# Optimization experiments

Hardware: AMD Instinct MI355X
Metric: run time of the kernel (lower is better)

Reference implementation:

```python
import jax, jax.numpy as jnp
import numpy as np

# Config (from Mamba3Config defaults)
D_MODEL = 768
EXPAND = 4
D_INNER = EXPAND * D_MODEL          # 3072
D_HEAD = 64
N_HEADS = D_INNER // D_HEAD         # 48
N_EXPERTS = 8
TOP_K = 2
R3 = 256                            # latent MoE input dim
R2 = 1024                           # latent MoE output dim
EPS = 1e-5
TANH_SCALE = 10.0                   # fast_scaled_tanh default
ROUTER_TEMP = 0.5                   # get_router_temperature(step=None) -> t_end


def _rms_norm(x, w):
    return x * jax.lax.rsqrt(jnp.mean(x * x, axis=-1, keepdims=True) + EPS) * w


def _scaled_tanh(x):
    return TANH_SCALE * jnp.tanh(x * (1.0 / TANH_SCALE))


def setup_inputs() -> dict:
    key = jax.random.key(0)
    ks = jax.random.split(key, 13)
    s = 0.02
    B, L = 2, 4096
    return {
        "x": jax.random.normal(ks[0], (B, L, D_MODEL), dtype=jnp.float32),
        "rms1_w": jnp.ones((D_MODEL,), jnp.float32),
        "W_in": s * jax.random.normal(ks[1], (D_MODEL, 2 * D_INNER + N_HEADS), jnp.float32),
        "dt_bias": jax.random.uniform(ks[2], (N_HEADS,), jnp.float32, -4.0, -1.0),  # dt in [dt_min, dt_max]-ish
        "W_out": s * jax.random.normal(ks[3], (D_INNER, D_MODEL), jnp.float32),
        "ls1": 0.01 * jnp.ones((D_MODEL,), jnp.float32),
        "rms2_w": jnp.ones((D_MODEL,), jnp.float32),
        "W_down": s * jax.random.normal(ks[4], (D_MODEL, R3), jnp.float32),
        "W_router": s * jax.random.normal(ks[5], (D_MODEL, N_EXPERTS), jnp.float32),
        "G": s * jax.random.normal(ks[6], (N_EXPERTS, R3, R2), jnp.float32),
        "W_up": s * jax.random.normal(ks[7], (R2, D_MODEL), jnp.float32),
        "ls2": 0.01 * jnp.ones((D_MODEL,), jnp.float32),
    }


def reference(x, rms1_w, W_in, dt_bias, W_out, ls1, rms2_w, W_down, W_router, G, W_up, ls2):
    B, L, _ = x.shape
    # ---- Mamba selective-scan branch ----
    xn = _rms_norm(x, rms1_w)
    proj = xn @ W_in                                   # [B,L,2*Di+H]
    u, z, dt = jnp.split(proj, [D_INNER, 2 * D_INNER], axis=-1)
    log_alpha = -jax.nn.softplus(dt + dt_bias)         # [B,L,H], per-head scalar decay
    alpha = jnp.exp(log_alpha)[..., None]              # [B,L,H,1]
    u4 = u.reshape(B, L, N_HEADS, D_HEAD)

    def combine(left, right):                          # first_order_combine_op
        a_l, b_l = left
        a_r, b_r = right
        return (a_r * a_l, a_r * b_l + b_r)

    _, h = jax.lax.associative_scan(
        combine, (jnp.broadcast_to(alpha, u4.shape), u4), axis=1)
    y = h.reshape(B, L, D_INNER) * jax.nn.silu(z)
    y = _scaled_tanh(y)
    x1 = x + ls1 * (y @ W_out)

    # ---- Fused latent MoE (Tucker) branch ----
    x2n = _rms_norm(x1, rms2_w)
    lat = _scaled_tanh(x2n @ W_down)                   # [B,L,r3]
    logits = (x2n @ W_router) * (1.0 / ROUTER_TEMP)    # [B,L,E]
    vals, idx = jax.lax.top_k(logits, TOP_K)
    probs = jax.nn.softmax(vals, axis=-1)              # [B,L,K]
    # dense combine weights: w[b,l,e] = sum_k probs_k * [idx_k == e]
    w = jnp.sum(jax.nn.one_hot(idx, N_EXPERTS, dtype=lat.dtype) * probs[..., None], axis=-2)
    # out[b,l,c] = sum_e w[b,l,e] * (lat[b,l,:] @ G[e])  (== fused gather grouped-GEMM)
    moe = jnp.einsum('blr,erc,ble->blc', lat, G, w)    # [B,L,r2]
    out = x1 + ls2 * (moe @ W_up)
    return out
```

## Files before the change

### kernel.cpp

```cpp
#include <hip/hip_runtime.h>
#include <stdint.h>

typedef unsigned short ushort_t;
typedef __attribute__((ext_vector_type(8))) __bf16 bf16x8;
typedef __attribute__((ext_vector_type(4))) float floatx4;
typedef __attribute__((ext_vector_type(8))) unsigned short ushort8v;

#define TT 8192L
#define LB 4096L
#define DD 768L
#define DI 3072L
#define NH 48L
#define R3C 256L
#define R2C 1024L
#define NP 6272L
#define CHS 64L

__device__ __forceinline__ float b2f(ushort_t u) {
  union { unsigned u32; float f; } v; v.u32 = ((unsigned)u) << 16; return v.f;
}
__device__ __forceinline__ ushort_t f2b(float f) {
  union { float f; unsigned u32; } v; v.f = f;
  unsigned r = v.u32 + 0x7FFFu + ((v.u32 >> 16) & 1u);
  return (ushort_t)(r >> 16);
}
__device__ __forceinline__ float fast_tanh(float x) {
  float e = __expf(2.0f * x);
  return 1.0f - 2.0f / (e + 1.0f);
}
__device__ __forceinline__ void g2l16(const void* g, void* l) {
  __builtin_amdgcn_global_load_lds(
      (const __attribute__((address_space(1))) unsigned int*)g,
      (__attribute__((address_space(3))) unsigned int*)l, 16, 0, 0);
}

__global__ __launch_bounds__(256) void k_prep(const float* __restrict__ s0, ushort_t* __restrict__ d0,
                                              const float* __restrict__ s1, ushort_t* __restrict__ d1,
                                              const float* __restrict__ s2, ushort_t* __restrict__ d2,
                                              const float* __restrict__ s3, ushort_t* __restrict__ d3,
                                              const float* __restrict__ s4, ushort_t* __restrict__ d4,
                                              const float* __restrict__ x,
                                              const float* __restrict__ w1,
                                              ushort_t* __restrict__ xn) {
  __shared__ float tile[64][65];
  int id = blockIdx.x;
  if (id < 2504) {
    const float* src; ushort_t* dst; int K, N, gx;
    if (id < 1176)      {            src = s0; dst = d0; K = 768;  N = 6192; gx = 12; }
    else if (id < 1752) { id -= 1176; src = s1; dst = d1; K = 3072; N = 768;  gx = 48; }
    else if (id < 1800) { id -= 1752; src = s2; dst = d2; K = 768;  N = 256;  gx = 12; }
    else if (id < 1992) { id -= 1800; src = s3; dst = d3; K = 1024; N = 768;  gx = 16; }
    else                { id -= 1992; src = s4; dst = d4; K = 2048; N = 1024; gx = 32; }
    int k0 = (id % gx) * 64, n0 = (id / gx) * 64;
    int c = threadIdx.x & 63, r4 = threadIdx.x >> 6;
#pragma unroll
    for (int s = 0; s < 16; s++) {
      int r = s * 4 + r4;
      int n = n0 + c;
      tile[c][r] = (n < N) ? src[(long)(k0 + r) * N + n] : 0.0f;
    }
    __syncthreads();
#pragma unroll
    for (int s = 0; s < 16; s++) {
      int r = s * 4 + r4;
      dst[(long)(n0 + r) * K + k0 + c] = f2b(tile[r][c]);
    }
  } else {
    int t = id - 2504, tid = threadIdx.x;
    int lane = tid & 63, wid = tid >> 6;
    const float* xr = x + (long)t * DD;
    float v0 = xr[tid], v1 = xr[tid + 256], v2 = xr[tid + 512];
    float ss = v0 * v0 + v1 * v1 + v2 * v2;
    for (int o = 32; o; o >>= 1) ss += __shfl_down(ss, o);
    __shared__ float red[4];
    if (lane == 0) red[wid] = ss;
    __syncthreads();
    float tot = red[0] + red[1] + red[2] + red[3];
    float rr = rsqrtf(tot / 768.0f + 1e-5f);
    ushort_t* orow = xn + (long)t * DD;
    orow[tid]       = f2b(v0 * rr * w1[tid]);
    orow[tid + 256] = f2b(v1 * rr * w1[tid + 256]);
    orow[tid + 512] = f2b(v2 * rr * w1[tid + 512]);
  }
}

__global__ __launch_bounds__(256) void k_fuse2(const float* __restrict__ P,
                                               const float* __restrict__ x,
                                               const float* __restrict__ ls1,
                                               const float* __restrict__ w2,
                                               const float* __restrict__ wr,
                                               ushort_t* __restrict__ x1,
                                               ushort_t* __restrict__ x2n,
                                               float* __restrict__ wrt) {
  int t = blockIdx.x, tid = threadIdx.x;
  int lane = tid & 63, wid = tid >> 6;
  int dd[3] = {tid, tid + 256, tid + 512};
  float v[3];
#pragma unroll
  for (int i = 0; i < 3; i++) {
    long ix = (long)t * DD + dd[i];
    float s = P[ix] + P[LB * DD + ix] + P[2 * LB * DD + ix] + P[3 * LB * DD + ix];
    float xv = x[ix] + ls1[dd[i]] * s;
    x1[ix] = f2b(xv);
    v[i] = xv;
  }
  float ss = v[0] * v[0] + v[1] * v[1] + v[2] * v[2];
  for (int o = 32; o; o >>= 1) ss += __shfl_down(ss, o);
  __shared__ float red[4];
  __shared__ float wred[4][8];
  __shared__ float slog[8];
  if (lane == 0) red[wid] = ss;
  __syncthreads();
  float tot = red[0] + red[1] + red[2] + red[3];
  float rr = rsqrtf(tot / 768.0f + 1e-5f);
  float p[8] = {0, 0, 0, 0, 0, 0, 0, 0};
  ushort_t* orow = x2n + (long)t * DD;
#pragma unroll
  for (int i = 0; i < 3; i++) {
    float xnv = v[i] * rr * w2[dd[i]];
    orow[dd[i]] = f2b(xnv);
    const float* wrow = wr + (long)dd[i] * 8;
#pragma unroll
    for (int e = 0; e < 8; e++) p[e] += xnv * wrow[e];
  }
#pragma unroll
  for (int e = 0; e < 8; e++) {
    float s = p[e];
    for (int o = 32; o; o >>= 1) s += __shfl_down(s, o);
    if (lane == 0) wred[wid][e] = s;
  }
  __syncthreads();
  if (tid < 8)
    slog[tid] = (wred[0][tid] + wred[1][tid] + wred[2][tid] + wred[3][tid]) * 2.0f;
  __syncthreads();
  if (tid == 0) {
    float l[8];
#pragma unroll
    for (int e = 0; e < 8; e++) l[e] = slog[e];
    int e0 = 0; float b0 = l[0];
#pragma unroll
    for (int e = 1; e < 8; e++) if (l[e] > b0) { b0 = l[e]; e0 = e; }
    int e1 = -1; float b1 = -1e30f;
#pragma unroll
    for (int e = 0; e < 8; e++) if (e != e0 && l[e] > b1) { b1 = l[e]; e1 = e; }
    float ex = __expf(b1 - b0);
    float pd = 1.0f / (1.0f + ex);
    float* wo = wrt + (long)t * 8;
#pragma unroll
    for (int e = 0; e < 8; e++) wo[e] = 0.0f;
    wo[e0] = pd;
    wo[e1] = ex * pd;
  }
}

__device__ __forceinline__ void stage_tile(const ushort_t* __restrict__ g, long rowstride,
                                           ushort_t* __restrict__ lds, int lane) {
  const int lrow = lane >> 3;
  const int dcol = (lane & 7) * 8;
#pragma unroll
  for (int c8 = 0; c8 < 8; c8++) {
    ushort8v v = *(const ushort8v*)(g + (long)(c8 * 8 + lrow) * rowstride + dcol);
    *(ushort8v*)&lds[(c8 * 64 + lane) * 8] = v;
  }
}

__device__ __forceinline__ float alpha_of(const ushort_t* __restrict__ proj, int tok, int h,
                                          const float* __restrict__ dtb) {
  float dt = b2f(proj[(long)tok * NP + 2 * DI + h]) + dtb[h];
  float sp = (dt > 20.0f) ? dt : log1pf(__expf(dt));
  return __expf(-sp);
}

__global__ __launch_bounds__(64) void k_scan1(const ushort_t* __restrict__ proj,
                                              const float* __restrict__ dtb,
                                              float* __restrict__ ssum,
                                              float* __restrict__ asum) {
  __shared__ __align__(16) ushort_t u_lds[64 * 64];
  __shared__ float s_alpha[64];
  const int lane = threadIdx.x;
  const int idx = blockIdx.x;
  const int c = idx & 63;
  const int h = idx >> 6;
  s_alpha[lane] = alpha_of(proj, (int)(c * CHS) + lane, h, dtb);
  const ushort_t* ug = proj + (long)c * CHS * NP + (long)h * 64;
  stage_tile(ug, NP, u_lds, lane);
  __syncthreads();
  float s = 0.0f, A = 1.0f;
#pragma unroll
  for (int tt = 0; tt < 64; tt++) {
    float a = s_alpha[tt];
    float u = b2f(u_lds[tt * 64 + lane]);
    s = fmaf(a, s, u);
    A *= a;
  }
  ssum[(long)idx * 64 + lane] = s;
  if (lane == 0) asum[idx] = A;
}

__global__ __launch_bounds__(64) void k_scan3(const ushort_t* __restrict__ proj,
                                              const float* __restrict__ dtb,
                                              const float* __restrict__ ssum,
                                              const float* __restrict__ asum,
                                              ushort_t* __restrict__ y) {
  __shared__ __align__(16) ushort_t u_lds[64 * 64];
  __shared__ __align__(16) ushort_t z_lds[64 * 64];
  __shared__ float s_alpha[64];
  const int lane = threadIdx.x;
  const int idx = blockIdx.x;
  const int c = idx & 63;
  const int h = idx >> 6;
  s_alpha[lane] = alpha_of(proj, (int)(c * CHS) + lane, h, dtb);
  const ushort_t* ug = proj + (long)c * CHS * NP + (long)h * 64;
  const ushort_t* zg = ug + DI;
  ushort_t* yg = y + (long)c * CHS * DI + (long)h * 64;
  stage_tile(ug, NP, u_lds, lane);
  stage_tile(zg, NP, z_lds, lane);
  float hs = 0.0f;
  for (int cc = 0; cc < c; cc++) {
    float A = asum[h * 64 + cc];
    float s = ssum[((long)(h * 64 + cc)) * 64 + lane];
    hs = fmaf(A, hs, s);
  }
  __syncthreads();
#pragma unroll
  for (int tt = 0; tt < 64; tt++) {
    float a = s_alpha[tt];
    float u = b2f(u_lds[tt * 64 + lane]);
    hs = fmaf(a, hs, u);
    float zv = b2f(z_lds[tt * 64 + lane]);
    float sig = 1.0f / (1.0f + __expf(-zv));
    float yv = hs * zv * sig;
    yv = 10.0f * fast_tanh(yv * 0.1f);
    yg[(long)tt * DI + lane] = f2b(yv);
  }
}

__global__ __launch_bounds__(256) void k_moe_in(const float* __restrict__ P,
                                                const float* __restrict__ wrt,
                                                ushort_t* __restrict__ abig) {
  int t = blockIdx.x, d = threadIdx.x;
  __shared__ float sw[8];
  if (d < 8) sw[d] = wrt[(long)t * 8 + d];
  long ix = (long)t * R3C + d;
  float s = P[ix] + P[TT * R3C + ix] + P[2 * TT * R3C + ix];
  __syncthreads();
  float lv = 10.0f * fast_tanh(0.1f * s);
  ushort_t* ab = abig + (long)t * 2048;
#pragma unroll
  for (int e = 0; e < 8; e++) ab[e * 256 + d] = f2b(sw[e] * lv);
}

template <int MODE>
__global__ __launch_bounds__(256, 4) void k_gemm(const ushort_t* __restrict__ A,
                                                 const ushort_t* __restrict__ Bt,
                                                 void* __restrict__ Cout, int K, int kstride,
                                                 int ldc, long zoff) {
  __shared__ __align__(16) ushort_t sA[2 * 128 * 32];
  __shared__ __align__(16) ushort_t sB[2 * 128 * 32];
  const int tid = threadIdx.x;
  const int lane = tid & 63, wid = tid >> 6;
  const int lm = lane & 15, q = lane >> 4;
  const int wm = wid >> 1, wn = wid & 1;
  const long row0 = (long)blockIdx.x * 128;
  const long col0 = (long)blockIdx.y * 128;
  const int z = blockIdx.z;
  A += (long)z * K;
  Bt += (long)z * K;

  floatx4 acc[4][4] = {};

  const int trow = tid >> 2;
  const int tcol = (tid & 3) * 8;
  const ushort_t* Ag = A + (row0 + trow) * (long)kstride + tcol;
  const ushort_t* Bg = Bt + (col0 + trow) * (long)kstride + tcol;
  const long rstep = 64L * kstride;

  for (int k0 = 0; k0 < K; k0 += 64) {
#pragma unroll
    for (int kk = 0; kk < 2; kk++)
#pragma unroll
      for (int rh = 0; rh < 2; rh++) {
        g2l16(Ag + rh * rstep + k0 + kk * 32, sA + kk * 4096 + rh * 2048 + wid * 512);
        g2l16(Bg + rh * rstep + k0 + kk * 32, sB + kk * 4096 + rh * 2048 + wid * 512);
      }
    __syncthreads();
#pragma unroll
    for (int kk = 0; kk < 2; kk++) {
      bf16x8 af[4], bfr[4];
#pragma unroll
      for (int i = 0; i < 4; i++)
        af[i] = *(const bf16x8*)(const void*)&sA[kk * 4096 + (wm * 64 + i * 16 + lm) * 32 + q * 8];
#pragma unroll
      for (int j = 0; j < 4; j++)
        bfr[j] = *(const bf16x8*)(const void*)&sB[kk * 4096 + (wn * 64 + j * 16 + lm) * 32 + q * 8];
#pragma unroll
      for (int i = 0; i < 4; i++)
#pragma unroll
        for (int j = 0; j < 4; j++)
          acc[i][j] = __builtin_amdgcn_mfma_f32_16x16x32_bf16(af[i], bfr[j], acc[i][j], 0, 0, 0);
    }
    __syncthreads();
  }

  if (MODE == 0) {
    ushort_t* ep = ((wid & 2) ? sB : sA) + (wid & 1) * 2304;
    ushort_t* Cb = (ushort_t*)Cout;
    const int rr = lane >> 3, cc = (lane & 7) * 8;
    __syncthreads();
#pragma unroll
    for (int p = 0; p < 2; p++) {
#pragma unroll
      for (int i2 = 0; i2 < 2; i2++)
#pragma unroll
        for (int j = 0; j < 4; j++)
#pragma unroll
          for (int r = 0; r < 4; r++)
            ep[(i2 * 16 + q * 4 + r) * 72 + j * 16 + lm] = f2b(acc[p * 2 + i2][j][r]);
#pragma unroll
      for (int s = 0; s < 4; s++) {
        ushort8v vv = *(const ushort8v*)&ep[(s * 8 + rr) * 72 + cc];
        long grow = row0 + wm * 64 + p * 32 + s * 8 + rr;
        *(ushort8v*)&Cb[grow * (long)ldc + col0 + wn * 64 + cc] = vv;
      }
    }
  } else {
#pragma unroll
    for (int i = 0; i < 4; i++) {
#pragma unroll
      for (int r = 0; r < 4; r++) {
        long row = row0 + wm * 64 + i * 16 + q * 4 + r;
#pragma unroll
        for (int j = 0; j < 4; j++) {
          long col = col0 + wn * 64 + j * 16 + lm;
          ((float*)Cout)[(long)z * zoff + row * (long)ldc + col] = acc[i][j][r];
        }
      }
    }
  }
}

__global__ __launch_bounds__(256) void k_comb_out(const float* __restrict__ P, long zoff, int nz,
                                                  const ushort_t* __restrict__ x1,
                                                  const float* __restrict__ ls,
                                                  float* __restrict__ outp) {
  long i = ((long)blockIdx.x * 256 + threadIdx.x) * 4;
  float s[4] = {0, 0, 0, 0};
  for (int zz = 0; zz < nz; zz++) {
    const float* p = P + (long)zz * zoff + i;
#pragma unroll
    for (int j = 0; j < 4; j++) s[j] += p[j];
  }
  int c = (int)(i % DD);
#pragma unroll
  for (int j = 0; j < 4; j++) outp[i + j] = b2f(x1[i + j]) + ls[c + j] * s[j];
}

#define OFF_WINT   0L
#define OFF_WOUTT  9633792L
#define OFF_WDNT   14352384L
#define OFF_WUPT   14745600L
#define OFF_GT     16318464L
#define OFF_X1     20512768L
#define OFF_WRT    33095680L
#define OFF_SSUM   34144256L
#define OFF_ASUM   34930688L
#define OFF_XN     35729408L
#define OFF_Y      48312320L
#define OFF_PROJ   73478144L
#define OFF_X2N    OFF_XN
#define OFF_PART   OFF_PROJ
#define OFF_DPART  OFF_Y
#define OFF_ABIG   OFF_PROJ
#define OFF_MOE    OFF_Y
#define OFF_UPART  OFF_PROJ
#define WS_NEEDED  124858368L

extern "C" void kernel_launch(void* const* d_in, const int* in_sizes, int n_in,
                              void* d_out, int out_size, void* d_ws, size_t ws_size,
                              hipStream_t stream) {
  const float* x     = (const float*)d_in[0];
  const float* rms1w = (const float*)d_in[1];
  const float* W_in  = (const float*)d_in[2];
  const float* dtb   = (const float*)d_in[3];
  const float* W_out = (const float*)d_in[4];
  const float* ls1   = (const float*)d_in[5];
  const float* rms2w = (const float*)d_in[6];
  const float* W_dn  = (const float*)d_in[7];
  const float* W_rtr = (const float*)d_in[8];
  const float* G     = (const float*)d_in[9];
  const float* W_up  = (const float*)d_in[10];
  const float* ls2   = (const float*)d_in[11];
  if (ws_size < (size_t)WS_NEEDED) return;

  char* ws = (char*)d_ws;
  ushort_t* W_inT  = (ushort_t*)(ws + OFF_WINT);
  ushort_t* W_outT = (ushort_t*)(ws + OFF_WOUTT);
  ushort_t* W_dnT  = (ushort_t*)(ws + OFF_WDNT);
  ushort_t* W_upT  = (ushort_t*)(ws + OFF_WUPT);
  ushort_t* GT     = (ushort_t*)(ws + OFF_GT);
  ushort_t* x1     = (ushort_t*)(ws + OFF_X1);
  float*    wrt    = (float*)(ws + OFF_WRT);
  float*    ssum   = (float*)(ws + OFF_SSUM);
  float*    asum   = (float*)(ws + OFF_ASUM);
  ushort_t* xn     = (ushort_t*)(ws + OFF_XN);
  ushort_t* y      = (ushort_t*)(ws + OFF_Y);
  ushort_t* proj   = (ushort_t*)(ws + OFF_PROJ);
  float*    part   = (float*)(ws + OFF_PART);
  float*    dpart  = (float*)(ws + OFF_DPART);
  ushort_t* abig   = (ushort_t*)(ws + OFF_ABIG);
  ushort_t* moe    = (ushort_t*)(ws + OFF_MOE);
  float*    upart  = (float*)(ws + OFF_UPART);
  ushort_t* x2n    = (ushort_t*)(ws + OFF_X2N);
  float*    outp   = (float*)d_out;

  k_prep<<<10696, 256, 0, stream>>>(W_in, W_inT, W_out, W_outT, W_dn, W_dnT,
                                    W_up, W_upT, G, GT, x, rms1w, xn);

  for (int b = 0; b < 2; b++) {
    const ushort_t* xnb = xn + (long)b * LB * DD;
    k_gemm<0><<<dim3(32, 49, 1), 256, 0, stream>>>(xnb, W_inT, proj, 768, 768, (int)NP, 0);
    k_scan1<<<3072, 64, 0, stream>>>(proj, dtb, ssum, asum);
    k_scan3<<<3072, 64, 0, stream>>>(proj, dtb, ssum, asum, y);
    k_gemm<4><<<dim3(32, 6, 4), 256, 0, stream>>>(y, W_outT, part, 768, 3072, 768, LB * DD);
    k_fuse2<<<4096, 256, 0, stream>>>(part, x + (long)b * LB * DD, ls1, rms2w, W_rtr,
                                      x1 + (long)b * LB * DD, x2n + (long)b * LB * DD,
                                      wrt + (long)b * LB * 8);
  }

  k_gemm<4><<<dim3(64, 2, 3), 256, 0, stream>>>(x2n, W_dnT, dpart, 256, 768, 256, TT * R3C);
  k_moe_in<<<8192, 256, 0, stream>>>(dpart, wrt, abig);
  k_gemm<0><<<dim3(64, 8, 1), 256, 0, stream>>>(abig, GT, moe, 2048, 2048, 1024, 0);
  k_gemm<4><<<dim3(64, 6, 2), 256, 0, stream>>>(moe, W_upT, upart, 512, 1024, 768, TT * DD);
  k_comb_out<<<6144, 256, 0, stream>>>(upart, TT * DD, 2, x1, ls2, outp);
}
```

Baseline: 534.0 us.

## Store split-K partials as bf16 and add a separate chunk-carry scan kernel

Split-K GEMM partial outputs are now written as bf16 through the LDS-staged vectorized epilogue instead of scattered fp32 stores, and the consumers (fuse2, moe_in, comb_out) read bf16. This halves partial-buffer traffic and gives coalesced stores. Separately, the per-block serial loop over earlier chunks in scan3, which costs O(c) work per block, is replaced by a small k_scan2 kernel that precomputes carries per head. Summing bf16-rounded partials loses some precision, and the change adds one extra launch per batch.

```diff
diff --git a/kernel.cpp b/kernel.cpp
--- a/kernel.cpp
+++ b/kernel.cpp
@@ -4,6 +4,7 @@
 typedef unsigned short ushort_t;
 typedef __attribute__((ext_vector_type(8))) __bf16 bf16x8;
 typedef __attribute__((ext_vector_type(4))) float floatx4;
+typedef __attribute__((ext_vector_type(4))) unsigned short ushort4v;
 typedef __attribute__((ext_vector_type(8))) unsigned short ushort8v;
 
 #define TT 8192L
@@ -84,7 +85,7 @@
   }
 }
 
-__global__ __launch_bounds__(256) void k_fuse2(const float* __restrict__ P,
+__global__ __launch_bounds__(256) void k_fuse2(const ushort_t* __restrict__ P,
                                                const float* __restrict__ x,
                                                const float* __restrict__ ls1,
                                                const float* __restrict__ w2,
@@ -99,7 +100,7 @@
 #pragma unroll
   for (int i = 0; i < 3; i++) {
     long ix = (long)t * DD + dd[i];
-    float s = P[ix] + P[LB * DD + ix] + P[2 * LB * DD + ix] + P[3 * LB * DD + ix];
+    float s = b2f(P[ix]) + b2f(P[LB * DD + ix]) + b2f(P[2 * LB * DD + ix]) + b2f(P[3 * LB * DD + ix]);
     float xv = x[ix] + ls1[dd[i]] * s;
     x1[ix] = f2b(xv);
     v[i] = xv;
@@ -197,10 +198,22 @@
   if (lane == 0) asum[idx] = A;
 }
 
+__global__ __launch_bounds__(64) void k_scan2(const float* __restrict__ ssum,
+                                              const float* __restrict__ asum,
+                                              float* __restrict__ carry) {
+  int h = blockIdx.x, lane = threadIdx.x;
+  float cv = 0.0f;
+  for (int c = 0; c < 64; c++) {
+    carry[((long)h * 64 + c) * 64 + lane] = cv;
+    float A = asum[h * 64 + c];
+    float s = ssum[((long)h * 64 + c) * 64 + lane];
+    cv = A * cv + s;
+  }
+}
+
 __global__ __launch_bounds__(64) void k_scan3(const ushort_t* __restrict__ proj,
                                               const float* __restrict__ dtb,
-                                              const float* __restrict__ ssum,
-                                              const float* __restrict__ asum,
+                                              const float* __restrict__ carry,
                                               ushort_t* __restrict__ y) {
   __shared__ __align__(16) ushort_t u_lds[64 * 64];
   __shared__ __align__(16) ushort_t z_lds[64 * 64];
@@ -215,13 +228,8 @@
   ushort_t* yg = y + (long)c * CHS * DI + (long)h * 64;
   stage_tile(ug, NP, u_lds, lane);
   stage_tile(zg, NP, z_lds, lane);
-  float hs = 0.0f;
-  for (int cc = 0; cc < c; cc++) {
-    float A = asum[h * 64 + cc];
-    float s = ssum[((long)(h * 64 + cc)) * 64 + lane];
-    hs = fmaf(A, hs, s);
-  }
-  __syncthreads();
+  __syncthreads();
+  float hs = carry[(long)idx * 64 + lane];
 #pragma unroll
   for (int tt = 0; tt < 64; tt++) {
     float a = s_alpha[tt];
@@ -235,14 +243,14 @@
   }
 }
 
-__global__ __launch_bounds__(256) void k_moe_in(const float* __restrict__ P,
+__global__ __launch_bounds__(256) void k_moe_in(const ushort_t* __restrict__ P,
                                                 const float* __restrict__ wrt,
                                                 ushort_t* __restrict__ abig) {
   int t = blockIdx.x, d = threadIdx.x;
   __shared__ float sw[8];
   if (d < 8) sw[d] = wrt[(long)t * 8 + d];
   long ix = (long)t * R3C + d;
-  float s = P[ix] + P[TT * R3C + ix] + P[2 * TT * R3C + ix];
+  float s = b2f(P[ix]) + b2f(P[TT * R3C + ix]) + b2f(P[2 * TT * R3C + ix]);
   __syncthreads();
   float lv = 10.0f * fast_tanh(0.1f * s);
   ushort_t* ab = abig + (long)t * 2048;
@@ -250,10 +258,9 @@
   for (int e = 0; e < 8; e++) ab[e * 256 + d] = f2b(sw[e] * lv);
 }
 
-template <int MODE>
 __global__ __launch_bounds__(256, 4) void k_gemm(const ushort_t* __restrict__ A,
                                                  const ushort_t* __restrict__ Bt,
-                                                 void* __restrict__ Cout, int K, int kstride,
+                                                 ushort_t* __restrict__ C, int K, int kstride,
                                                  int ldc, long zoff) {
   __shared__ __align__(16) ushort_t sA[2 * 128 * 32];
   __shared__ __align__(16) ushort_t sB[2 * 128 * 32];
@@ -302,53 +309,37 @@
     __syncthreads();
   }
 
-  if (MODE == 0) {
-    ushort_t* ep = ((wid & 2) ? sB : sA) + (wid & 1) * 2304;
-    ushort_t* Cb = (ushort_t*)Cout;
-    const int rr = lane >> 3, cc = (lane & 7) * 8;
-    __syncthreads();
-#pragma unroll
-    for (int p = 0; p < 2; p++) {
-#pragma unroll
-      for (int i2 = 0; i2 < 2; i2++)
-#pragma unroll
-        for (int j = 0; j < 4; j++)
-#pragma unroll
-          for (int r = 0; r < 4; r++)
-            ep[(i2 * 16 + q * 4 + r) * 72 + j * 16 + lm] = f2b(acc[p * 2 + i2][j][r]);
-#pragma unroll
-      for (int s = 0; s < 4; s++) {
-        ushort8v vv = *(const ushort8v*)&ep[(s * 8 + rr) * 72 + cc];
-        long grow = row0 + wm * 64 + p * 32 + s * 8 + rr;
-        *(ushort8v*)&Cb[grow * (long)ldc + col0 + wn * 64 + cc] = vv;
-      }
+  ushort_t* ep = ((wid & 2) ? sB : sA) + (wid & 1) * 2304;
+  ushort_t* Cb = C + (long)z * zoff;
+  const int rr = lane >> 3, cc = (lane & 7) * 8;
+  __syncthreads();
+#pragma unroll
+  for (int p = 0; p < 2; p++) {
+#pragma unroll
+    for (int i2 = 0; i2 < 2; i2++)
+#pragma unroll
+      for (int j = 0; j < 4; j++)
+#pragma unroll
+        for (int r = 0; r < 4; r++)
+          ep[(i2 * 16 + q * 4 + r) * 72 + j * 16 + lm] = f2b(acc[p * 2 + i2][j][r]);
+#pragma unroll
+    for (int s = 0; s < 4; s++) {
+      ushort8v vv = *(const ushort8v*)&ep[(s * 8 + rr) * 72 + cc];
+      long grow = row0 + wm * 64 + p * 32 + s * 8 + rr;
+      *(ushort8v*)&Cb[grow * (long)ldc + col0 + wn * 64 + cc] = vv;
     }
-  } else {
-#pragma unroll
-    for (int i = 0; i < 4; i++) {
-#pragma unroll
-      for (int r = 0; r < 4; r++) {
-        long row = row0 + wm * 64 + i * 16 + q * 4 + r;
-#pragma unroll
-        for (int j = 0; j < 4; j++) {
-          long col = col0 + wn * 64 + j * 16 + lm;
-          ((float*)Cout)[(long)z * zoff + row * (long)ldc + col] = acc[i][j][r];
-        }
-      }
-    }
-  }
-}
-
-__global__ __launch_bounds__(256) void k_comb_out(const float* __restrict__ P, long zoff, int nz,
+  }
+}
+
+__global__ __launch_bounds__(256) void k_comb_out(const ushort_t* __restrict__ P, long zoff, int nz,
                                                   const ushort_t* __restrict__ x1,
                                                   const float* __restrict__ ls,
                                                   float* __restrict__ outp) {
   long i = ((long)blockIdx.x * 256 + threadIdx.x) * 4;
   float s[4] = {0, 0, 0, 0};
   for (int zz = 0; zz < nz; zz++) {
-    const float* p = P + (long)zz * zoff + i;
-#pragma unroll
-    for (int j = 0; j < 4; j++) s[j] += p[j];
+    ushort4v pv = *(const ushort4v*)(P + (long)zz * zoff + i);
+    s[0] += b2f(pv.x); s[1] += b2f(pv.y); s[2] += b2f(pv.z); s[3] += b2f(pv.w);
   }
   int c = (int)(i % DD);
 #pragma unroll
@@ -364,6 +355,7 @@
 #define OFF_WRT    33095680L
 #define OFF_SSUM   34144256L
 #define OFF_ASUM   34930688L
+#define OFF_CARRY  34942976L
 #define OFF_XN     35729408L
 #define OFF_Y      48312320L
 #define OFF_PROJ   73478144L
@@ -402,14 +394,15 @@
   float*    wrt    = (float*)(ws + OFF_WRT);
   float*    ssum   = (float*)(ws + OFF_SSUM);
   float*    asum   = (float*)(ws + OFF_ASUM);
+  float*    carry  = (float*)(ws + OFF_CARRY);
   ushort_t* xn     = (ushort_t*)(ws + OFF_XN);
   ushort_t* y      = (ushort_t*)(ws + OFF_Y);
   ushort_t* proj   = (ushort_t*)(ws + OFF_PROJ);
-  float*    part   = (float*)(ws + OFF_PART);
-  float*    dpart  = (float*)(ws + OFF_DPART);
+  ushort_t* part   = (ushort_t*)(ws + OFF_PART);
+  ushort_t* dpart  = (ushort_t*)(ws + OFF_DPART);
   ushort_t* abig   = (ushort_t*)(ws + OFF_ABIG);
   ushort_t* moe    = (ushort_t*)(ws + OFF_MOE);
-  float*    upart  = (float*)(ws + OFF_UPART);
+  ushort_t* upart  = (ushort_t*)(ws + OFF_UPART);
   ushort_t* x2n    = (ushort_t*)(ws + OFF_X2N);
   float*    outp   = (float*)d_out;
 
@@ -418,18 +411,19 @@
 
   for (int b = 0; b < 2; b++) {
     const ushort_t* xnb = xn + (long)b * LB * DD;
-    k_gemm<0><<<dim3(32, 49, 1), 256, 0, stream>>>(xnb, W_inT, proj, 768, 768, (int)NP, 0);
+    k_gemm<<<dim3(32, 49, 1), 256, 0, stream>>>(xnb, W_inT, proj, 768, 768, (int)NP, 0);
     k_scan1<<<3072, 64, 0, stream>>>(proj, dtb, ssum, asum);
-    k_scan3<<<3072, 64, 0, stream>>>(proj, dtb, ssum, asum, y);
-    k_gemm<4><<<dim3(32, 6, 4), 256, 0, stream>>>(y, W_outT, part, 768, 3072, 768, LB * DD);
+    k_scan2<<<48, 64, 0, stream>>>(ssum, asum, carry);
+    k_scan3<<<3072, 64, 0, stream>>>(proj, dtb, carry, y);
+    k_gemm<<<dim3(32, 6, 4), 256, 0, stream>>>(y, W_outT, part, 768, 3072, 768, LB * DD);
     k_fuse2<<<4096, 256, 0, stream>>>(part, x + (long)b * LB * DD, ls1, rms2w, W_rtr,
                                       x1 + (long)b * LB * DD, x2n + (long)b * LB * DD,
                                       wrt + (long)b * LB * 8);
   }
 
-  k_gemm<4><<<dim3(64, 2, 3), 256, 0, stream>>>(x2n, W_dnT, dpart, 256, 768, 256, TT * R3C);
+  k_gemm<<<dim3(64, 2, 3), 256, 0, stream>>>(x2n, W_dnT, dpart, 256, 768, 256, TT * R3C);
   k_moe_in<<<8192, 256, 0, stream>>>(dpart, wrt, abig);
-  k_gemm<0><<<dim3(64, 8, 1), 256, 0, stream>>>(abig, GT, moe, 2048, 2048, 1024, 0);
-  k_gemm<4><<<dim3(64, 6, 2), 256, 0, stream>>>(moe, W_upT, upart, 512, 1024, 768, TT * DD);
+  k_gemm<<<dim3(64, 8, 1), 256, 0, stream>>>(abig, GT, moe, 2048, 2048, 1024, 0);
+  k_gemm<<<dim3(64, 6, 2), 256, 0, stream>>>(moe, W_upT, upart, 512, 1024, 768, TT * DD);
   k_comb_out<<<6144, 256, 0, stream>>>(upart, TT * DD, 2, x1, ls2, outp);
 }
```

After: 495.7 us. 7.2% less time.
